# Kernel tuning notes

Hardware: AMD Instinct MI355X
Metric: run time of the kernel (lower is better)

## Reference

```python
import jax, jax.numpy as jnp
import numpy as np

N_NODES = 50000
N_EDGES = 800000
IN_CH, HIDDEN, OUT_CH = 64, 16, 8


def setup_inputs() -> dict:
    key = jax.random.key(0)
    ks = jax.random.split(key, 8)
    x = jax.random.normal(ks[0], (N_NODES, IN_CH), dtype=jnp.float32)
    edge_index = jax.random.randint(ks[1], (2, N_EDGES), 0, N_NODES, dtype=jnp.int64)
    # SAGEConv params: lin_l (neighbor aggregate, has bias), lin_r (root, no bias)
    s1 = 1.0 / np.sqrt(IN_CH)
    s2 = 1.0 / np.sqrt(HIDDEN)
    W1l = jax.random.uniform(ks[2], (HIDDEN, IN_CH), jnp.float32, -s1, s1)
    W1r = jax.random.uniform(ks[3], (HIDDEN, IN_CH), jnp.float32, -s1, s1)
    b1 = jax.random.uniform(ks[4], (HIDDEN,), jnp.float32, -s1, s1)
    W2l = jax.random.uniform(ks[5], (OUT_CH, HIDDEN), jnp.float32, -s2, s2)
    W2r = jax.random.uniform(ks[6], (OUT_CH, HIDDEN), jnp.float32, -s2, s2)
    b2 = jax.random.uniform(ks[7], (OUT_CH,), jnp.float32, -s2, s2)
    return {"x": x, "W1l": W1l, "W1r": W1r, "b1": b1,
            "W2l": W2l, "W2r": W2r, "b2": b2, "edge_index": edge_index}


def _sage_conv(x, src, dst, Wl, Wr, b, n_nodes):
    # mean-aggregate neighbor features: gather from src, scatter-mean to dst
    msg_sum = jax.ops.segment_sum(x[src], dst, num_segments=n_nodes)  # [N, d]
    deg = jax.ops.segment_sum(jnp.ones((src.shape[0], 1), x.dtype), dst,
                              num_segments=n_nodes)                    # [N, 1]
    aggr = msg_sum / jnp.maximum(deg, 1.0)
    # out = lin_l(aggr) + lin_r(x); bias lives in lin_l
    return aggr @ Wl.T + x @ Wr.T + b


def reference(x, W1l, W1r, b1, W2l, W2r, b2, edge_index):
    src, dst = edge_index[0], edge_index[1]
    n = x.shape[0]
    h = jax.nn.relu(_sage_conv(x, src, dst, W1l, W1r, b1, n))
    # F.dropout(p=0.1, training=self.training): identity in eval mode
    return _sage_conv(h, src, dst, W2l, W2r, b2, n)
```

## Files before the change

kernel.cpp:

```cpp
#include <hip/hip_runtime.h>

#define IN_CH 64
#define HID   16
#define OUTC  8
#define BINSHIFT 6
#define BINCAP  (1 << BINSHIFT)
#define CHUNK   2048

typedef _Float16 half2_t __attribute__((ext_vector_type(2)));
typedef _Float16 half4_t __attribute__((ext_vector_type(4)));


__global__ __launch_bounds__(256) void build_xform(
    const float* __restrict__ x,
    const int*   __restrict__ esrc,
    const int*   __restrict__ edst,
    const float* __restrict__ W1l,
    const float* __restrict__ W1r,
    const float* __restrict__ b1,
    int* __restrict__ cur,
    unsigned short* __restrict__ adj,
    _Float16* __restrict__ y1h,
    float* __restrict__ r1,
    int n_nodes, int n_edges, int nb_scatter)
{
    __shared__ __align__(16) float sWl[HID * 68];
    __shared__ __align__(16) float sWr[HID * 68];
    __shared__ __align__(16) float sx[16 * 68];
    __shared__ float sb1[HID];

    int b   = blockIdx.x;
    int tid = threadIdx.x;

    if (b < nb_scatter) {
        int slice = b & 7;
        int chunk = b >> 3;
        int lo = (int)(((long long)slice       * n_nodes) >> 3);
        int hi = (int)(((long long)(slice + 1) * n_nodes) >> 3);
        int base = chunk * CHUNK;
#pragma unroll
        for (int j = 0; j < CHUNK / 256; ++j) {
            int e = base + j * 256 + tid;
            if (e < n_edges) {
                int d = edst[e];
                if (d >= lo && d < hi) {
                    int pos = atomicAdd(&cur[d], 1);
                    if (pos < BINCAP)
                        adj[((size_t)d << BINSHIFT) + pos] =
                            (unsigned short)esrc[e];
                }
            }
        }
        return;
    }

    for (int i = tid; i < HID * IN_CH; i += 256) {
        int c = i >> 6, k = i & 63;
        sWl[c * 68 + k] = W1l[i];
        sWr[c * 68 + k] = W1r[i];
    }
    if (tid < HID) sb1[tid] = b1[tid];

    int nl   = tid >> 4;
    int c    = tid & 15;
    int node = (b - nb_scatter) * 16 + nl;

    if (node < n_nodes)
        *(float4*)&sx[nl * 68 + c * 4] =
            *(const float4*)&x[(size_t)node * IN_CH + c * 4];
    __syncthreads();
    if (node >= n_nodes) return;

    float accL = 0.f, accR = 0.f;
#pragma unroll
    for (int k4 = 0; k4 < 16; ++k4) {
        float4 xv = *(const float4*)&sx [nl * 68 + k4 * 4];
        float4 wl = *(const float4*)&sWl[c  * 68 + k4 * 4];
        float4 wr = *(const float4*)&sWr[c  * 68 + k4 * 4];
        accL = fmaf(xv.x, wl.x, accL); accL = fmaf(xv.y, wl.y, accL);
        accL = fmaf(xv.z, wl.z, accL); accL = fmaf(xv.w, wl.w, accL);
        accR = fmaf(xv.x, wr.x, accR); accR = fmaf(xv.y, wr.y, accR);
        accR = fmaf(xv.z, wr.z, accR); accR = fmaf(xv.w, wr.w, accR);
    }
    y1h[(size_t)node * HID + c] = (_Float16)accL;
    r1 [(size_t)node * HID + c] = accR + sb1[c];
}

__global__ __launch_bounds__(256) void fused_gather(
    const float* __restrict__ r1,
    const _Float16* __restrict__ y1h,
    const int*   __restrict__ cur,
    const unsigned short* __restrict__ adj,
    const float* __restrict__ W2l, const float* __restrict__ W2r,
    const float* __restrict__ b2,
    _Float16* __restrict__ y2h, float* __restrict__ r2out,
    int n_nodes)
{
    __shared__ float sW2l[HID * OUTC];
    __shared__ float sW2r[HID * OUTC];
    __shared__ float sb2[OUTC];
    __shared__ float sh[64 * 17];

    int tid = threadIdx.x;
    for (int i = tid; i < HID * OUTC; i += 256) {
        int o = i >> 4, k = i & 15;
        sW2l[k * OUTC + o] = W2l[i];
        sW2r[k * OUTC + o] = W2r[i];
    }
    if (tid < OUTC) sb2[tid] = b2[tid];

    int nl   = tid >> 2;
    int q    = tid & 3;
    int node = blockIdx.x * 64 + nl;
    bool real = node < n_nodes;

    const half2_t k10 = {(_Float16)1.f, (_Float16)0.f};
    const half2_t k01 = {(_Float16)0.f, (_Float16)1.f};

    if (real) {
        int deg = cur[node];
        if (deg > BINCAP) deg = BINCAP;
        int iters = deg >> 2;
        float s0 = 0.f, s1 = 0.f, s2 = 0.f, s3 = 0.f;
        const _Float16* yq = y1h + q * 4;
        const unsigned short* row = adj + ((size_t)node << BINSHIFT);
        const ushort4* ap = (const ushort4*)row;
        for (int it = 0; it < iters; ++it) {
            ushort4 s = ap[it];
            half4_t v0 = *(const half4_t*)(yq + (size_t)s.x * HID);
            half4_t v1 = *(const half4_t*)(yq + (size_t)s.y * HID);
            half4_t v2 = *(const half4_t*)(yq + (size_t)s.z * HID);
            half4_t v3 = *(const half4_t*)(yq + (size_t)s.w * HID);
            half2_t v0l = {v0.x, v0.y}, v0h = {v0.z, v0.w};
            half2_t v1l = {v1.x, v1.y}, v1h = {v1.z, v1.w};
            half2_t v2l = {v2.x, v2.y}, v2h = {v2.z, v2.w};
            half2_t v3l = {v3.x, v3.y}, v3h = {v3.z, v3.w};
            s0 = __builtin_amdgcn_fdot2(v0l, k10, s0, false);
            s1 = __builtin_amdgcn_fdot2(v0l, k01, s1, false);
            s2 = __builtin_amdgcn_fdot2(v0h, k10, s2, false);
            s3 = __builtin_amdgcn_fdot2(v0h, k01, s3, false);
            s0 = __builtin_amdgcn_fdot2(v1l, k10, s0, false);
            s1 = __builtin_amdgcn_fdot2(v1l, k01, s1, false);
            s2 = __builtin_amdgcn_fdot2(v1h, k10, s2, false);
            s3 = __builtin_amdgcn_fdot2(v1h, k01, s3, false);
            s0 = __builtin_amdgcn_fdot2(v2l, k10, s0, false);
            s1 = __builtin_amdgcn_fdot2(v2l, k01, s1, false);
            s2 = __builtin_amdgcn_fdot2(v2h, k10, s2, false);
            s3 = __builtin_amdgcn_fdot2(v2h, k01, s3, false);
            s0 = __builtin_amdgcn_fdot2(v3l, k10, s0, false);
            s1 = __builtin_amdgcn_fdot2(v3l, k01, s1, false);
            s2 = __builtin_amdgcn_fdot2(v3h, k10, s2, false);
            s3 = __builtin_amdgcn_fdot2(v3h, k01, s3, false);
        }
        for (int g = iters << 2; g < deg; ++g) {
            half4_t v = *(const half4_t*)(yq + (size_t)row[g] * HID);
            half2_t vl = {v.x, v.y}, vh = {v.z, v.w};
            s0 = __builtin_amdgcn_fdot2(vl, k10, s0, false);
            s1 = __builtin_amdgcn_fdot2(vl, k01, s1, false);
            s2 = __builtin_amdgcn_fdot2(vh, k10, s2, false);
            s3 = __builtin_amdgcn_fdot2(vh, k01, s3, false);
        }
        float inv = 1.0f / fmaxf((float)deg, 1.0f);
        float4 rv = *(const float4*)&r1[(size_t)node * HID + q * 4];
        sh[nl * 17 + q * 4 + 0] = fmaxf(fmaf(s0, inv, rv.x), 0.f);
        sh[nl * 17 + q * 4 + 1] = fmaxf(fmaf(s1, inv, rv.y), 0.f);
        sh[nl * 17 + q * 4 + 2] = fmaxf(fmaf(s2, inv, rv.z), 0.f);
        sh[nl * 17 + q * 4 + 3] = fmaxf(fmaf(s3, inv, rv.w), 0.f);
    }
    __syncthreads();
    if (!real) return;

    const float* hrow = &sh[nl * 17];
    if (q < 2) {
        int ob = q * 4;
        float a0 = 0.f, a1 = 0.f, a2 = 0.f, a3 = 0.f;
#pragma unroll
        for (int k = 0; k < HID; ++k) {
            float hv = hrow[k];
            a0 = fmaf(hv, sW2l[k * OUTC + ob + 0], a0);
            a1 = fmaf(hv, sW2l[k * OUTC + ob + 1], a1);
            a2 = fmaf(hv, sW2l[k * OUTC + ob + 2], a2);
            a3 = fmaf(hv, sW2l[k * OUTC + ob + 3], a3);
        }
        half4_t o;
        o.x = (_Float16)a0; o.y = (_Float16)a1;
        o.z = (_Float16)a2; o.w = (_Float16)a3;
        *(half4_t*)(y2h + (size_t)node * OUTC + ob) = o;
    } else {
        int ob = (q - 2) * 4;
        float a0 = sb2[ob + 0], a1 = sb2[ob + 1];
        float a2 = sb2[ob + 2], a3 = sb2[ob + 3];
#pragma unroll
        for (int k = 0; k < HID; ++k) {
            float hv = hrow[k];
            a0 = fmaf(hv, sW2r[k * OUTC + ob + 0], a0);
            a1 = fmaf(hv, sW2r[k * OUTC + ob + 1], a1);
            a2 = fmaf(hv, sW2r[k * OUTC + ob + 2], a2);
            a3 = fmaf(hv, sW2r[k * OUTC + ob + 3], a3);
        }
        float4 o = {a0, a1, a2, a3};
        *(float4*)(r2out + (size_t)node * OUTC + ob) = o;
    }
}

__global__ __launch_bounds__(256) void gather_out(
    const _Float16* __restrict__ y2h,
    const int*   __restrict__ cur,
    const unsigned short* __restrict__ adj,
    float* __restrict__ out,
    int n_nodes)
{
    int tid = threadIdx.x;
    int node = blockIdx.x * 128 + (tid >> 1);
    if (node >= n_nodes) return;
    int r = tid & 1;

    int deg = cur[node];
    if (deg > BINCAP) deg = BINCAP;
    int iters = deg >> 2;
    const _Float16* yq = y2h + r * 4;
    const unsigned short* row = adj + ((size_t)node << BINSHIFT);
    const ushort4* ap = (const ushort4*)row;

    const half2_t k10 = {(_Float16)1.f, (_Float16)0.f};
    const half2_t k01 = {(_Float16)0.f, (_Float16)1.f};

    float s0 = 0.f, s1 = 0.f, s2 = 0.f, s3 = 0.f;
    for (int it = 0; it < iters; ++it) {
        ushort4 s = ap[it];
        half4_t v0 = *(const half4_t*)(yq + (size_t)s.x * OUTC);
        half4_t v1 = *(const half4_t*)(yq + (size_t)s.y * OUTC);
        half4_t v2 = *(const half4_t*)(yq + (size_t)s.z * OUTC);
        half4_t v3 = *(const half4_t*)(yq + (size_t)s.w * OUTC);
        half2_t v0l = {v0.x, v0.y}, v0h = {v0.z, v0.w};
        half2_t v1l = {v1.x, v1.y}, v1h = {v1.z, v1.w};
        half2_t v2l = {v2.x, v2.y}, v2h = {v2.z, v2.w};
        half2_t v3l = {v3.x, v3.y}, v3h = {v3.z, v3.w};
        s0 = __builtin_amdgcn_fdot2(v0l, k10, s0, false);
        s1 = __builtin_amdgcn_fdot2(v0l, k01, s1, false);
        s2 = __builtin_amdgcn_fdot2(v0h, k10, s2, false);
        s3 = __builtin_amdgcn_fdot2(v0h, k01, s3, false);
        s0 = __builtin_amdgcn_fdot2(v1l, k10, s0, false);
        s1 = __builtin_amdgcn_fdot2(v1l, k01, s1, false);
        s2 = __builtin_amdgcn_fdot2(v1h, k10, s2, false);
        s3 = __builtin_amdgcn_fdot2(v1h, k01, s3, false);
        s0 = __builtin_amdgcn_fdot2(v2l, k10, s0, false);
        s1 = __builtin_amdgcn_fdot2(v2l, k01, s1, false);
        s2 = __builtin_amdgcn_fdot2(v2h, k10, s2, false);
        s3 = __builtin_amdgcn_fdot2(v2h, k01, s3, false);
        s0 = __builtin_amdgcn_fdot2(v3l, k10, s0, false);
        s1 = __builtin_amdgcn_fdot2(v3l, k01, s1, false);
        s2 = __builtin_amdgcn_fdot2(v3h, k10, s2, false);
        s3 = __builtin_amdgcn_fdot2(v3h, k01, s3, false);
    }
    for (int g = iters << 2; g < deg; ++g) {
        half4_t v = *(const half4_t*)(yq + (size_t)row[g] * OUTC);
        half2_t vl = {v.x, v.y}, vh = {v.z, v.w};
        s0 = __builtin_amdgcn_fdot2(vl, k10, s0, false);
        s1 = __builtin_amdgcn_fdot2(vl, k01, s1, false);
        s2 = __builtin_amdgcn_fdot2(vh, k10, s2, false);
        s3 = __builtin_amdgcn_fdot2(vh, k01, s3, false);
    }
    float inv = 1.0f / fmaxf((float)deg, 1.0f);

    float4* op = (float4*)(out + (size_t)node * OUTC + r * 4);
    float4 cv = *op;
    cv.x = fmaf(s0, inv, cv.x);
    cv.y = fmaf(s1, inv, cv.y);
    cv.z = fmaf(s2, inv, cv.z);
    cv.w = fmaf(s3, inv, cv.w);
    *op = cv;
}

extern "C" void kernel_launch(void* const* d_in, const int* in_sizes, int n_in,
                              void* d_out, int out_size, void* d_ws, size_t ws_size,
                              hipStream_t stream)
{
    const float* x   = (const float*)d_in[0];
    const float* W1l = (const float*)d_in[1];
    const float* W1r = (const float*)d_in[2];
    const float* b1  = (const float*)d_in[3];
    const float* W2l = (const float*)d_in[4];
    const float* W2r = (const float*)d_in[5];
    const float* b2  = (const float*)d_in[6];
    const int*   ei  = (const int*)d_in[7];

    int n_nodes = in_sizes[0] / IN_CH;
    int n_edges = in_sizes[7] / 2;
    const int* esrc = ei;
    const int* edst = ei + n_edges;

    float* out = (float*)d_out;

    char* wsb = (char*)d_ws;
    _Float16* y1h = (_Float16*)wsb;
    _Float16* y2h = y1h + (size_t)n_nodes * HID;
    float* r1 = (float*)(y2h + (size_t)n_nodes * OUTC);
    int* cur  = (int*)(r1 + (size_t)n_nodes * HID);
    unsigned short* adj = (unsigned short*)(cur + n_nodes);

    dim3 blk(256);
    int n_chunks   = (n_edges + CHUNK - 1) / CHUNK;
    int nb_scatter = n_chunks * 8;
    int nb_node    = (n_nodes + 15) / 16;

    hipMemsetAsync(cur, 0, (size_t)n_nodes * sizeof(int), stream);

    build_xform<<<dim3(nb_scatter + nb_node), blk, 0, stream>>>(
        x, esrc, edst, W1l, W1r, b1, cur, adj, y1h, r1,
        n_nodes, n_edges, nb_scatter);

    fused_gather<<<dim3((n_nodes + 63) / 64), blk, 0, stream>>>(
        r1, y1h, cur, adj, W2l, W2r, b2, y2h, out, n_nodes);

    gather_out<<<dim3((n_nodes + 127) / 128), blk, 0, stream>>>(
        y2h, cur, adj, out, n_nodes);
}
```

Measured before the change: 135.7 us.

## Use persistent XCC-affine scatter blocks with atomic work queues per node slice

Replaces the fixed one-block-per-(chunk,slice) scatter grid with 768 persistent blocks. Each block reads its XCC id and first drains chunks from the atomic queue of its own node slice, then moves on to the other slices. The intent is to keep cur/adj atomics for a slice mostly on one XCC's L2, which improves cache locality, and to cut block launch overhead. In exchange it adds per-chunk global atomics and two __syncthreads per chunk. It also depends on XCC ids lining up with slice ownership, which the hardware does not guarantee.

```diff
diff --git a/kernel.cpp b/kernel.cpp
--- a/kernel.cpp
+++ b/kernel.cpp
@@ -19,35 +19,48 @@
     const float* __restrict__ W1r,
     const float* __restrict__ b1,
     int* __restrict__ cur,
+    int* __restrict__ q,
     unsigned short* __restrict__ adj,
     _Float16* __restrict__ y1h,
     float* __restrict__ r1,
-    int n_nodes, int n_edges, int nb_scatter)
+    int n_nodes, int n_edges, int n_chunks, int nb_scatter)
 {
     __shared__ __align__(16) float sWl[HID * 68];
     __shared__ __align__(16) float sWr[HID * 68];
     __shared__ __align__(16) float sx[16 * 68];
     __shared__ float sb1[HID];
+    __shared__ int sChunk;
 
     int b   = blockIdx.x;
     int tid = threadIdx.x;
 
     if (b < nb_scatter) {
-        int slice = b & 7;
-        int chunk = b >> 3;
-        int lo = (int)(((long long)slice       * n_nodes) >> 3);
-        int hi = (int)(((long long)(slice + 1) * n_nodes) >> 3);
-        int base = chunk * CHUNK;
+        int xcc;
+        asm("s_getreg_b32 %0, hwreg(HW_REG_XCC_ID)" : "=s"(xcc));
+        xcc &= 7;
+        for (int p = 0; p < 8; ++p) {
+            int s  = (xcc + p) & 7;
+            int lo = (int)(((long long)s       * n_nodes) >> 3);
+            int hi = (int)(((long long)(s + 1) * n_nodes) >> 3);
+            while (true) {
+                __syncthreads();
+                if (tid == 0) sChunk = atomicAdd(&q[s], 1);
+                __syncthreads();
+                int chunk = sChunk;
+                if (chunk >= n_chunks) break;
+                int base = chunk * CHUNK;
 #pragma unroll
-        for (int j = 0; j < CHUNK / 256; ++j) {
-            int e = base + j * 256 + tid;
-            if (e < n_edges) {
-                int d = edst[e];
-                if (d >= lo && d < hi) {
-                    int pos = atomicAdd(&cur[d], 1);
-                    if (pos < BINCAP)
-                        adj[((size_t)d << BINSHIFT) + pos] =
-                            (unsigned short)esrc[e];
+                for (int j = 0; j < CHUNK / 256; ++j) {
+                    int e = base + j * 256 + tid;
+                    if (e < n_edges) {
+                        int d = edst[e];
+                        if (d >= lo && d < hi) {
+                            int pos = atomicAdd(&cur[d], 1);
+                            if (pos < BINCAP)
+                                adj[((size_t)d << BINSHIFT) + pos] =
+                                    (unsigned short)esrc[e];
+                        }
+                    }
                 }
             }
         }
@@ -297,18 +310,19 @@
     _Float16* y2h = y1h + (size_t)n_nodes * HID;
     float* r1 = (float*)(y2h + (size_t)n_nodes * OUTC);
     int* cur  = (int*)(r1 + (size_t)n_nodes * HID);
-    unsigned short* adj = (unsigned short*)(cur + n_nodes);
+    int* q    = cur + n_nodes;
+    unsigned short* adj = (unsigned short*)(q + 8);
 
     dim3 blk(256);
     int n_chunks   = (n_edges + CHUNK - 1) / CHUNK;
-    int nb_scatter = n_chunks * 8;
+    int nb_scatter = 768;
     int nb_node    = (n_nodes + 15) / 16;
 
-    hipMemsetAsync(cur, 0, (size_t)n_nodes * sizeof(int), stream);
+    hipMemsetAsync(cur, 0, ((size_t)n_nodes + 8) * sizeof(int), stream);
 
     build_xform<<<dim3(nb_scatter + nb_node), blk, 0, stream>>>(
-        x, esrc, edst, W1l, W1r, b1, cur, adj, y1h, r1,
-        n_nodes, n_edges, nb_scatter);
+        x, esrc, edst, W1l, W1r, b1, cur, q, adj, y1h, r1,
+        n_nodes, n_edges, n_chunks, nb_scatter);
 
     fused_gather<<<dim3((n_nodes + 63) / 64), blk, 0, stream>>>(
         r1, y1h, cur, adj, W2l, W2r, b2, y2h, out, n_nodes);
```

New measurement: 220.5 us. 1.62x slower.

## Split each node's neighbor list across four lanes with shuffle reduction

Applied to the files above, without the earlier changes.

Both gather kernels now split each node's edge list across four extra lanes, which stride through the ushort4 index groups and combine their partial sums with xor shuffles. This shortens the serial dependent-load chain per thread, exposing more memory-level parallelism for average degree around 16. In exchange it launches four times more threads, adds shuffle reductions, leaves three of four lanes idle in the epilogue, and narrows the second-layer matmul to one output per thread.

```diff
diff --git a/kernel.cpp b/kernel.cpp
--- a/kernel.cpp
+++ b/kernel.cpp
@@ -99,7 +99,7 @@
     __shared__ float sW2l[HID * OUTC];
     __shared__ float sW2r[HID * OUTC];
     __shared__ float sb2[OUTC];
-    __shared__ float sh[64 * 17];
+    __shared__ float sh[16 * 17];
 
     int tid = threadIdx.x;
     for (int i = tid; i < HID * OUTC; i += 256) {
@@ -109,9 +109,11 @@
     }
     if (tid < OUTC) sb2[tid] = b2[tid];
 
-    int nl   = tid >> 2;
-    int q    = tid & 3;
-    int node = blockIdx.x * 64 + nl;
+    int nl   = tid >> 4;
+    int t    = tid & 15;
+    int q    = t >> 2;
+    int ep   = t & 3;
+    int node = blockIdx.x * 16 + nl;
     bool real = node < n_nodes;
 
     const half2_t k10 = {(_Float16)1.f, (_Float16)0.f};
@@ -125,7 +127,7 @@
         const _Float16* yq = y1h + q * 4;
         const unsigned short* row = adj + ((size_t)node << BINSHIFT);
         const ushort4* ap = (const ushort4*)row;
-        for (int it = 0; it < iters; ++it) {
+        for (int it = ep; it < iters; it += 4) {
             ushort4 s = ap[it];
             half4_t v0 = *(const half4_t*)(yq + (size_t)s.x * HID);
             half4_t v1 = *(const half4_t*)(yq + (size_t)s.y * HID);
@@ -152,7 +154,7 @@
             s2 = __builtin_amdgcn_fdot2(v3h, k10, s2, false);
             s3 = __builtin_amdgcn_fdot2(v3h, k01, s3, false);
         }
-        for (int g = iters << 2; g < deg; ++g) {
+        for (int g = (iters << 2) + ep; g < deg; g += 4) {
             half4_t v = *(const half4_t*)(yq + (size_t)row[g] * HID);
             half2_t vl = {v.x, v.y}, vh = {v.z, v.w};
             s0 = __builtin_amdgcn_fdot2(vl, k10, s0, false);
@@ -160,46 +162,37 @@
             s2 = __builtin_amdgcn_fdot2(vh, k10, s2, false);
             s3 = __builtin_amdgcn_fdot2(vh, k01, s3, false);
         }
-        float inv = 1.0f / fmaxf((float)deg, 1.0f);
-        float4 rv = *(const float4*)&r1[(size_t)node * HID + q * 4];
-        sh[nl * 17 + q * 4 + 0] = fmaxf(fmaf(s0, inv, rv.x), 0.f);
-        sh[nl * 17 + q * 4 + 1] = fmaxf(fmaf(s1, inv, rv.y), 0.f);
-        sh[nl * 17 + q * 4 + 2] = fmaxf(fmaf(s2, inv, rv.z), 0.f);
-        sh[nl * 17 + q * 4 + 3] = fmaxf(fmaf(s3, inv, rv.w), 0.f);
+        s0 += __shfl_xor(s0, 1); s0 += __shfl_xor(s0, 2);
+        s1 += __shfl_xor(s1, 1); s1 += __shfl_xor(s1, 2);
+        s2 += __shfl_xor(s2, 1); s2 += __shfl_xor(s2, 2);
+        s3 += __shfl_xor(s3, 1); s3 += __shfl_xor(s3, 2);
+
+        if (ep == 0) {
+            float inv = 1.0f / fmaxf((float)deg, 1.0f);
+            float4 rv = *(const float4*)&r1[(size_t)node * HID + q * 4];
+            sh[nl * 17 + q * 4 + 0] = fmaxf(fmaf(s0, inv, rv.x), 0.f);
+            sh[nl * 17 + q * 4 + 1] = fmaxf(fmaf(s1, inv, rv.y), 0.f);
+            sh[nl * 17 + q * 4 + 2] = fmaxf(fmaf(s2, inv, rv.z), 0.f);
+            sh[nl * 17 + q * 4 + 3] = fmaxf(fmaf(s3, inv, rv.w), 0.f);
+        }
     }
     __syncthreads();
     if (!real) return;
 
     const float* hrow = &sh[nl * 17];
-    if (q < 2) {
-        int ob = q * 4;
-        float a0 = 0.f, a1 = 0.f, a2 = 0.f, a3 = 0.f;
+    if (t < OUTC) {
+        float a = 0.f;
 #pragma unroll
-        for (int k = 0; k < HID; ++k) {
-            float hv = hrow[k];
-            a0 = fmaf(hv, sW2l[k * OUTC + ob + 0], a0);
-            a1 = fmaf(hv, sW2l[k * OUTC + ob + 1], a1);
-            a2 = fmaf(hv, sW2l[k * OUTC + ob + 2], a2);
-            a3 = fmaf(hv, sW2l[k * OUTC + ob + 3], a3);
-        }
-        half4_t o;
-        o.x = (_Float16)a0; o.y = (_Float16)a1;
-        o.z = (_Float16)a2; o.w = (_Float16)a3;
-        *(half4_t*)(y2h + (size_t)node * OUTC + ob) = o;
+        for (int k = 0; k < HID; ++k)
+            a = fmaf(hrow[k], sW2l[k * OUTC + t], a);
+        y2h[(size_t)node * OUTC + t] = (_Float16)a;
     } else {
-        int ob = (q - 2) * 4;
-        float a0 = sb2[ob + 0], a1 = sb2[ob + 1];
-        float a2 = sb2[ob + 2], a3 = sb2[ob + 3];
+        int o = t - OUTC;
+        float a = sb2[o];
 #pragma unroll
-        for (int k = 0; k < HID; ++k) {
-            float hv = hrow[k];
-            a0 = fmaf(hv, sW2r[k * OUTC + ob + 0], a0);
-            a1 = fmaf(hv, sW2r[k * OUTC + ob + 1], a1);
-            a2 = fmaf(hv, sW2r[k * OUTC + ob + 2], a2);
-            a3 = fmaf(hv, sW2r[k * OUTC + ob + 3], a3);
-        }
-        float4 o = {a0, a1, a2, a3};
-        *(float4*)(r2out + (size_t)node * OUTC + ob) = o;
+        for (int k = 0; k < HID; ++k)
+            a = fmaf(hrow[k], sW2r[k * OUTC + o], a);
+        r2out[(size_t)node * OUTC + o] = a;
     }
 }
 
@@ -210,10 +203,12 @@
     float* __restrict__ out,
     int n_nodes)
 {
-    int tid = threadIdx.x;
-    int node = blockIdx.x * 128 + (tid >> 1);
+    int tid  = threadIdx.x;
+    int node = blockIdx.x * 32 + (tid >> 3);
     if (node >= n_nodes) return;
-    int r = tid & 1;
+    int t  = tid & 7;
+    int r  = t >> 2;
+    int ep = t & 3;
 
     int deg = cur[node];
     if (deg > BINCAP) deg = BINCAP;
@@ -226,7 +221,7 @@
     const half2_t k01 = {(_Float16)0.f, (_Float16)1.f};
 
     float s0 = 0.f, s1 = 0.f, s2 = 0.f, s3 = 0.f;
-    for (int it = 0; it < iters; ++it) {
+    for (int it = ep; it < iters; it += 4) {
         ushort4 s = ap[it];
         half4_t v0 = *(const half4_t*)(yq + (size_t)s.x * OUTC);
         half4_t v1 = *(const half4_t*)(yq + (size_t)s.y * OUTC);
@@ -253,7 +248,7 @@
         s2 = __builtin_amdgcn_fdot2(v3h, k10, s2, false);
         s3 = __builtin_amdgcn_fdot2(v3h, k01, s3, false);
     }
-    for (int g = iters << 2; g < deg; ++g) {
+    for (int g = (iters << 2) + ep; g < deg; g += 4) {
         half4_t v = *(const half4_t*)(yq + (size_t)row[g] * OUTC);
         half2_t vl = {v.x, v.y}, vh = {v.z, v.w};
         s0 = __builtin_amdgcn_fdot2(vl, k10, s0, false);
@@ -261,8 +256,13 @@
         s2 = __builtin_amdgcn_fdot2(vh, k10, s2, false);
         s3 = __builtin_amdgcn_fdot2(vh, k01, s3, false);
     }
+    s0 += __shfl_xor(s0, 1); s0 += __shfl_xor(s0, 2);
+    s1 += __shfl_xor(s1, 1); s1 += __shfl_xor(s1, 2);
+    s2 += __shfl_xor(s2, 1); s2 += __shfl_xor(s2, 2);
+    s3 += __shfl_xor(s3, 1); s3 += __shfl_xor(s3, 2);
+    if (ep != 0) return;
+
     float inv = 1.0f / fmaxf((float)deg, 1.0f);
-
     float4* op = (float4*)(out + (size_t)node * OUTC + r * 4);
     float4 cv = *op;
     cv.x = fmaf(s0, inv, cv.x);
@@ -310,9 +310,9 @@
         x, esrc, edst, W1l, W1r, b1, cur, adj, y1h, r1,
         n_nodes, n_edges, nb_scatter);
 
-    fused_gather<<<dim3((n_nodes + 63) / 64), blk, 0, stream>>>(
+    fused_gather<<<dim3((n_nodes + 15) / 16), blk, 0, stream>>>(
         r1, y1h, cur, adj, W2l, W2r, b2, y2h, out, n_nodes);
 
-    gather_out<<<dim3((n_nodes + 127) / 128), blk, 0, stream>>>(
+    gather_out<<<dim3((n_nodes + 31) / 32), blk, 0, stream>>>(
         y2h, cur, adj, out, n_nodes);
 }
```

Result: no change. 134.9 us (-0.6%).
